# Kernel optimization log

Measured on AMD Instinct MI355X. Metric: run time of the kernel, lower is better.

Reference implementation:

```python
import jax, jax.numpy as jnp
import numpy as np

EPS = 1e-4  # ProtoPNet epsilon in distance-to-similarity transform


def setup_inputs() -> dict:
    key = jax.random.key(0)
    k1, k2, k3 = jax.random.split(key, 3)
    B, C, T = 128, 128, 777   # backbone feature map [B, C, T]
    P, NC = 500, 5            # prototypes, classes
    x = jax.random.normal(k1, (B, C, T), dtype=jnp.float32)
    prototypes = jax.random.uniform(k2, (P, C), dtype=jnp.float32)
    last_w = jax.random.normal(k3, (P, NC), dtype=jnp.float32)
    return {"x": x, "prototypes": prototypes, "last_w": last_w}


def reference(x, prototypes, last_w):
    # Prototype layer via the conv-trick L2 expansion:
    x2 = jnp.sum(x * x, axis=1)                      # [B, T]
    p2 = jnp.sum(prototypes * prototypes, axis=1)    # [P]
    xp = jnp.einsum('bct,pc->bpt', x, prototypes)    # [B, P, T]  (dominant GEMM)
    d = jnp.maximum(x2[:, None, :] - 2.0 * xp + p2[None, :, None], 0.0)  # [B, P, T]
    # Min-pool over all patches (global min over temporal axis)
    min_d = jnp.min(d, axis=2)                       # [B, P]
    # Distance -> similarity: log((d + 1) / (d + eps))
    sim = jnp.log((min_d + 1.0) / (min_d + EPS))     # [B, P]
    # Final evidence layer
    logits = sim @ last_w                            # [B, num_classes]
    return logits
```

## Files before the change

### kernel.cpp

```cpp
#include <hip/hip_runtime.h>
#include <hip/hip_bf16.h>

#define B_DIM 128
#define C_DIM 128
#define T_DIM 777
#define T_PAD 832
#define P_DIM 500
#define P_PAD 512
#define NCLS  5
#define EPSV  1e-4f

typedef unsigned short u16;
typedef __attribute__((ext_vector_type(8))) short short8;
typedef __attribute__((ext_vector_type(4))) float f32x4;

__device__ __forceinline__ u16 f2bf(float f) {
    unsigned u = __float_as_uint(f);
    u += 0x7FFFu + ((u >> 16) & 1u);
    return (u16)(u >> 16);
}

__global__ __launch_bounds__(256) void prep_x(const float* __restrict__ x,
                                              u16* __restrict__ xbf,
                                              float* __restrict__ x2) {
    const int tc = blockIdx.x;
    const int b  = blockIdx.y;
    const int tid = threadIdx.x, w = tid >> 6, l = tid & 63;
    __shared__ __align__(16) u16 xt[64][136];
    const int t_loc = w * 16 + (l & 15);
    const int cg = l >> 4;
    const int t = tc * 64 + t_loc;
    const float* xb = x + (size_t)b * C_DIM * T_DIM;
    float acc = 0.f;
#pragma unroll 8
    for (int c0 = 0; c0 < C_DIM; c0 += 4) {
        int c = c0 + cg;
        float v = (t < T_DIM) ? xb[c * T_DIM + t] : 0.f;
        acc = fmaf(v, v, acc);
        xt[t_loc][c] = f2bf(v);
    }
    acc += __shfl_xor(acc, 16);
    acc += __shfl_xor(acc, 32);
    if (cg == 0) x2[b * T_PAD + t] = (t < T_DIM) ? acc : 1e30f;
    __syncthreads();
    int4* dst = (int4*)(xbf + ((size_t)b * T_PAD + tc * 64) * C_DIM);
#pragma unroll
    for (int q = 0; q < 4; ++q) {
        int f = q * 256 + tid;
        int tr = f >> 4, g = f & 15;
        dst[f] = *(const int4*)((const char*)xt + tr * 272 + g * 16);
    }
}

__global__ void prep_p2(const float* __restrict__ proto, float* __restrict__ p2) {
    int p = blockIdx.x * 64 + threadIdx.x;
    float a = 0.f;
    if (p < P_DIM) {
        const float* pr = proto + p * C_DIM;
#pragma unroll 8
        for (int c = 0; c < C_DIM; ++c) { float v = pr[c]; a = fmaf(v, v, a); }
    }
    p2[p] = (p < P_DIM) ? a : 0.f;
}

__global__ __launch_bounds__(256, 2) void gemm_min(const u16* __restrict__ xbf,
                                                   const float* __restrict__ x2,
                                                   const float* __restrict__ proto,
                                                   const float* __restrict__ p2ws,
                                                   float* __restrict__ simws) {
    const int o = blockIdx.x;
    const int xcd = o & 7, j = o >> 3;
    const int b = xcd * 16 + (j >> 2);
    const int pt = j & 3;
    const int tid = threadIdx.x, w = tid >> 6, l = tid & 63;
    const int wp = pt * 128 + w * 32;
    const int row16 = l & 15, kq = l >> 4;

    __shared__ __align__(16) char smem[32 * 256];

    short8 afr[2][4];
#pragma unroll
    for (int ps = 0; ps < 2; ++ps) {
        int r = wp + ps * 16 + row16;
#pragma unroll
        for (int kst = 0; kst < 4; ++kst) {
            int k0 = kst * 32 + kq * 8;
            float f[8];
            if (r < P_DIM) {
                float4 u0 = *(const float4*)(proto + r * C_DIM + k0);
                float4 u1 = *(const float4*)(proto + r * C_DIM + k0 + 4);
                f[0]=u0.x; f[1]=u0.y; f[2]=u0.z; f[3]=u0.w;
                f[4]=u1.x; f[5]=u1.y; f[6]=u1.z; f[7]=u1.w;
            } else {
#pragma unroll
                for (int q = 0; q < 8; ++q) f[q] = 0.f;
            }
            short8 s;
#pragma unroll
            for (int q = 0; q < 8; ++q) s[q] = (short)f2bf(f[q]);
            afr[ps][kst] = s;
        }
    }
    float p2r[2][4];
#pragma unroll
    for (int ps = 0; ps < 2; ++ps)
#pragma unroll
        for (int q = 0; q < 4; ++q) p2r[ps][q] = p2ws[wp + ps * 16 + kq * 4 + q];

    const int4* xg = (const int4*)xbf;
    const size_t base_g = (size_t)b * T_PAD * 16;
    const int f0 = tid, f1 = tid + 256;
    const int tl0 = f0 >> 4, g0 = f0 & 15;
    const int tl1 = f1 >> 4, g1 = f1 & 15;
    char* wr0 = smem + tl0 * 256 + ((g0 ^ (tl0 & 7)) << 4);
    char* wr1 = smem + tl1 * 256 + ((g1 ^ (tl1 & 7)) << 4);
    int4 v0 = xg[base_g + (size_t)tl0 * 16 + g0];
    int4 v1 = xg[base_g + (size_t)tl1 * 16 + g1];

    float minv[2][4];
#pragma unroll
    for (int ps = 0; ps < 2; ++ps)
#pragma unroll
        for (int q = 0; q < 4; ++q) minv[ps][q] = 1e30f;

    const float* x2b = x2 + b * T_PAD;

    for (int it = 0; it < T_PAD / 32; ++it) {
        *(int4*)wr0 = v0;
        *(int4*)wr1 = v1;
        if (it + 1 < T_PAD / 32) {
            v0 = xg[base_g + (size_t)((it + 1) * 32 + tl0) * 16 + g0];
            v1 = xg[base_g + (size_t)((it + 1) * 32 + tl1) * 16 + g1];
        }
        __syncthreads();

        f32x4 acc[2][2];
#pragma unroll
        for (int ps = 0; ps < 2; ++ps)
#pragma unroll
            for (int ts = 0; ts < 2; ++ts) acc[ps][ts] = (f32x4){0.f, 0.f, 0.f, 0.f};

#pragma unroll
        for (int kst = 0; kst < 4; ++kst) {
            short8 bfr[2];
#pragma unroll
            for (int ts = 0; ts < 2; ++ts) {
                int tl = ts * 16 + row16;
                int gr = (kst * 4 + kq) ^ (tl & 7);
                bfr[ts] = *(const short8*)(smem + tl * 256 + (gr << 4));
            }
#pragma unroll
            for (int ps = 0; ps < 2; ++ps)
#pragma unroll
                for (int ts = 0; ts < 2; ++ts)
                    acc[ps][ts] = __builtin_amdgcn_mfma_f32_16x16x32_bf16(
                        afr[ps][kst], bfr[ts], acc[ps][ts], 0, 0, 0);
        }
        float x2v0 = x2b[it * 32 + row16];
        float x2v1 = x2b[it * 32 + 16 + row16];
#pragma unroll
        for (int ps = 0; ps < 2; ++ps)
#pragma unroll
            for (int q = 0; q < 4; ++q) {
                minv[ps][q] = fminf(minv[ps][q], fmaf(-2.f, acc[ps][0][q], x2v0));
                minv[ps][q] = fminf(minv[ps][q], fmaf(-2.f, acc[ps][1][q], x2v1));
            }
        __syncthreads();
    }

#pragma unroll
    for (int m = 1; m <= 8; m <<= 1)
#pragma unroll
        for (int ps = 0; ps < 2; ++ps)
#pragma unroll
            for (int q = 0; q < 4; ++q)
                minv[ps][q] = fminf(minv[ps][q], __shfl_xor(minv[ps][q], m));

    if (row16 == 0) {
#pragma unroll
        for (int ps = 0; ps < 2; ++ps)
#pragma unroll
            for (int q = 0; q < 4; ++q) {
                int p = wp + ps * 16 + kq * 4 + q;
                if (p < P_DIM) {
                    float md = fmaxf(minv[ps][q] + p2r[ps][q], 0.f);
                    simws[b * P_PAD + p] = logf((md + 1.f) / (md + EPSV));
                }
            }
    }
}

__global__ void logits_k(const float* __restrict__ simws, const float* __restrict__ lw,
                         float* __restrict__ out) {
    int b = blockIdx.x, l = threadIdx.x;
    float a[NCLS] = {0.f, 0.f, 0.f, 0.f, 0.f};
    for (int p = l; p < P_DIM; p += 64) {
        float s = simws[b * P_PAD + p];
#pragma unroll
        for (int n = 0; n < NCLS; ++n) a[n] = fmaf(s, lw[p * NCLS + n], a[n]);
    }
#pragma unroll
    for (int m = 1; m <= 32; m <<= 1)
#pragma unroll
        for (int n = 0; n < NCLS; ++n) a[n] += __shfl_xor(a[n], m);
    if (l == 0) {
#pragma unroll
        for (int n = 0; n < NCLS; ++n) out[b * NCLS + n] = a[n];
    }
}

__global__ __launch_bounds__(256) void fallback_k(const float* __restrict__ x,
                                                  const float* __restrict__ proto,
                                                  const float* __restrict__ lw,
                                                  float* __restrict__ out) {
    __shared__ float x2s[T_DIM];
    __shared__ float sims[P_DIM];
    int b = blockIdx.x, tid = threadIdx.x;
    for (int t = tid; t < T_DIM; t += 256) {
        float a = 0.f;
        for (int c = 0; c < C_DIM; ++c) { float v = x[((size_t)b * C_DIM + c) * T_DIM + t]; a = fmaf(v, v, a); }
        x2s[t] = a;
    }
    __syncthreads();
    for (int p = tid; p < P_DIM; p += 256) {
        float p2 = 0.f;
        for (int c = 0; c < C_DIM; ++c) { float v = proto[p * C_DIM + c]; p2 = fmaf(v, v, p2); }
        float mind = 1e30f;
        for (int t = 0; t < T_DIM; ++t) {
            float xp = 0.f;
            for (int c = 0; c < C_DIM; ++c)
                xp = fmaf(x[((size_t)b * C_DIM + c) * T_DIM + t], proto[p * C_DIM + c], xp);
            float d = fmaxf(x2s[t] - 2.f * xp + p2, 0.f);
            mind = fminf(mind, d);
        }
        sims[p] = logf((mind + 1.f) / (mind + EPSV));
    }
    __syncthreads();
    if (tid < NCLS) {
        float a = 0.f;
        for (int p = 0; p < P_DIM; ++p) a = fmaf(sims[p], lw[p * NCLS + tid], a);
        out[b * NCLS + tid] = a;
    }
}

extern "C" void kernel_launch(void* const* d_in, const int* in_sizes, int n_in,
                              void* d_out, int out_size, void* d_ws, size_t ws_size,
                              hipStream_t stream) {
    const float* x     = (const float*)d_in[0];
    const float* proto = (const float*)d_in[1];
    const float* lw    = (const float*)d_in[2];
    float* out = (float*)d_out;

    const size_t xbf_bytes = (size_t)B_DIM * T_PAD * C_DIM * 2;
    const size_t x2_off  = xbf_bytes;
    const size_t p2_off  = x2_off + (size_t)B_DIM * T_PAD * 4;
    const size_t sim_off = p2_off + (size_t)P_PAD * 4;
    const size_t need    = sim_off + (size_t)B_DIM * P_PAD * 4;

    if (ws_size >= need) {
        u16*   xbf = (u16*)d_ws;
        float* x2  = (float*)((char*)d_ws + x2_off);
        float* p2  = (float*)((char*)d_ws + p2_off);
        float* sim = (float*)((char*)d_ws + sim_off);
        prep_x  <<<dim3(T_PAD / 64, B_DIM), 256, 0, stream>>>(x, xbf, x2);
        prep_p2 <<<dim3(P_PAD / 64),        64,  0, stream>>>(proto, p2);
        gemm_min<<<dim3(512),               256, 0, stream>>>(xbf, x2, proto, p2, sim);
        logits_k<<<dim3(B_DIM),             64,  0, stream>>>(sim, lw, out);
    } else {
        fallback_k<<<dim3(B_DIM), 256, 0, stream>>>(x, proto, lw, out);
    }
}
```

Before: 51.64 us.

## Fuse x bf16 conversion and norms into GEMM-min, split T across blocks

Removes the separate prep_x pass, which wrote a bf16 transposed copy of x plus x2 to workspace. The GEMM kernel now loads fp32 x directly, computes the squared norms and bf16-converts into shared memory itself. Each block now covers 256 prototypes and half of the T range, so two partial minima per (b,p) are combined in the logits kernel, which also computes the prototype norms. The goal is to cut launches and the global round-trip of the converted x, at the cost of more register pressure and per-iteration conversion and shuffle work inside the GEMM loop.

After: 43.15 us. 16.4% less time.

```diff
diff --git a/kernel.cpp b/kernel.cpp
--- a/kernel.cpp
+++ b/kernel.cpp
@@ -4,87 +4,56 @@
 #define B_DIM 128
 #define C_DIM 128
 #define T_DIM 777
-#define T_PAD 832
 #define P_DIM 500
 #define P_PAD 512
 #define NCLS  5
 #define EPSV  1e-4f
+#define NT    25
 
 typedef unsigned short u16;
+typedef unsigned int   u32;
 typedef __attribute__((ext_vector_type(8))) short short8;
 typedef __attribute__((ext_vector_type(4))) float f32x4;
+typedef float float4u __attribute__((ext_vector_type(4), aligned(4)));
 
 __device__ __forceinline__ u16 f2bf(float f) {
-    unsigned u = __float_as_uint(f);
+    u32 u = __float_as_uint(f);
     u += 0x7FFFu + ((u >> 16) & 1u);
     return (u16)(u >> 16);
 }
 
-__global__ __launch_bounds__(256) void prep_x(const float* __restrict__ x,
-                                              u16* __restrict__ xbf,
-                                              float* __restrict__ x2) {
-    const int tc = blockIdx.x;
-    const int b  = blockIdx.y;
-    const int tid = threadIdx.x, w = tid >> 6, l = tid & 63;
-    __shared__ __align__(16) u16 xt[64][136];
-    const int t_loc = w * 16 + (l & 15);
-    const int cg = l >> 4;
-    const int t = tc * 64 + t_loc;
-    const float* xb = x + (size_t)b * C_DIM * T_DIM;
-    float acc = 0.f;
-#pragma unroll 8
-    for (int c0 = 0; c0 < C_DIM; c0 += 4) {
-        int c = c0 + cg;
-        float v = (t < T_DIM) ? xb[c * T_DIM + t] : 0.f;
-        acc = fmaf(v, v, acc);
-        xt[t_loc][c] = f2bf(v);
-    }
-    acc += __shfl_xor(acc, 16);
-    acc += __shfl_xor(acc, 32);
-    if (cg == 0) x2[b * T_PAD + t] = (t < T_DIM) ? acc : 1e30f;
-    __syncthreads();
-    int4* dst = (int4*)(xbf + ((size_t)b * T_PAD + tc * 64) * C_DIM);
-#pragma unroll
-    for (int q = 0; q < 4; ++q) {
-        int f = q * 256 + tid;
-        int tr = f >> 4, g = f & 15;
-        dst[f] = *(const int4*)((const char*)xt + tr * 272 + g * 16);
-    }
-}
-
-__global__ void prep_p2(const float* __restrict__ proto, float* __restrict__ p2) {
-    int p = blockIdx.x * 64 + threadIdx.x;
-    float a = 0.f;
-    if (p < P_DIM) {
-        const float* pr = proto + p * C_DIM;
-#pragma unroll 8
-        for (int c = 0; c < C_DIM; ++c) { float v = pr[c]; a = fmaf(v, v, a); }
-    }
-    p2[p] = (p < P_DIM) ? a : 0.f;
-}
-
-__global__ __launch_bounds__(256, 2) void gemm_min(const u16* __restrict__ xbf,
-                                                   const float* __restrict__ x2,
-                                                   const float* __restrict__ proto,
-                                                   const float* __restrict__ p2ws,
-                                                   float* __restrict__ simws) {
+__global__ __launch_bounds__(256, 2) void fused_gemm_min(
+    const float* __restrict__ x,
+    const float* __restrict__ proto,
+    float* __restrict__ wsmin) {
+
     const int o = blockIdx.x;
     const int xcd = o & 7, j = o >> 3;
-    const int b = xcd * 16 + (j >> 2);
-    const int pt = j & 3;
-    const int tid = threadIdx.x, w = tid >> 6, l = tid & 63;
-    const int wp = pt * 128 + w * 32;
+    const int b   = xcd * 16 + (j >> 2);
+    const int pt  = (j >> 1) & 1, th = j & 1;
+    const int it0 = th ? 13 : 0;
+    const int itN = th ? NT : 13;
+
+    const int tid = threadIdx.x;
+    const int w = tid >> 6, l = tid & 63;
     const int row16 = l & 15, kq = l >> 4;
-
-    __shared__ __align__(16) char smem[32 * 256];
-
-    short8 afr[2][4];
-#pragma unroll
-    for (int ps = 0; ps < 2; ++ps) {
-        int r = wp + ps * 16 + row16;
+    const int wp = pt * 256 + w * 64;
+
+    const int c0  = (tid >> 3) << 2;
+    const int tl0 = (tid & 7) << 2;
+
+    __shared__ __align__(16) char  smem[32 * 256];
+    __shared__ __align__(16) float x2p[4][32];
+
+    const float* xb = x + (size_t)b * C_DIM * T_DIM;
+
+    short8 afr[4][4];
+#pragma unroll
+    for (int ps = 0; ps < 4; ++ps) {
+        const int r = wp + ps * 16 + row16;
 #pragma unroll
         for (int kst = 0; kst < 4; ++kst) {
-            int k0 = kst * 32 + kq * 8;
+            const int k0 = kst * 32 + kq * 8;
             float f[8];
             if (r < P_DIM) {
                 float4 u0 = *(const float4*)(proto + r * C_DIM + k0);
@@ -95,48 +64,76 @@
 #pragma unroll
                 for (int q = 0; q < 8; ++q) f[q] = 0.f;
             }
-            short8 s;
-#pragma unroll
-            for (int q = 0; q < 8; ++q) s[q] = (short)f2bf(f[q]);
-            afr[ps][kst] = s;
-        }
-    }
-    float p2r[2][4];
-#pragma unroll
-    for (int ps = 0; ps < 2; ++ps)
-#pragma unroll
-        for (int q = 0; q < 4; ++q) p2r[ps][q] = p2ws[wp + ps * 16 + kq * 4 + q];
-
-    const int4* xg = (const int4*)xbf;
-    const size_t base_g = (size_t)b * T_PAD * 16;
-    const int f0 = tid, f1 = tid + 256;
-    const int tl0 = f0 >> 4, g0 = f0 & 15;
-    const int tl1 = f1 >> 4, g1 = f1 & 15;
-    char* wr0 = smem + tl0 * 256 + ((g0 ^ (tl0 & 7)) << 4);
-    char* wr1 = smem + tl1 * 256 + ((g1 ^ (tl1 & 7)) << 4);
-    int4 v0 = xg[base_g + (size_t)tl0 * 16 + g0];
-    int4 v1 = xg[base_g + (size_t)tl1 * 16 + g1];
-
-    float minv[2][4];
-#pragma unroll
-    for (int ps = 0; ps < 2; ++ps)
-#pragma unroll
-        for (int q = 0; q < 4; ++q) minv[ps][q] = 1e30f;
-
-    const float* x2b = x2 + b * T_PAD;
-
-    for (int it = 0; it < T_PAD / 32; ++it) {
-        *(int4*)wr0 = v0;
-        *(int4*)wr1 = v1;
-        if (it + 1 < T_PAD / 32) {
-            v0 = xg[base_g + (size_t)((it + 1) * 32 + tl0) * 16 + g0];
-            v1 = xg[base_g + (size_t)((it + 1) * 32 + tl1) * 16 + g1];
+            short8 s8;
+#pragma unroll
+            for (int q = 0; q < 8; ++q) s8[q] = (short)f2bf(f[q]);
+            afr[ps][kst] = s8;
+        }
+    }
+
+    float vb[4][4];
+    auto loadv = [&](int it) {
+        const int tb = it * 32 + tl0;
+        if (tb + 3 < T_DIM) {
+#pragma unroll
+            for (int r = 0; r < 4; ++r) {
+                float4u u = *(const float4u*)(xb + (c0 + r) * T_DIM + tb);
+                vb[r][0]=u[0]; vb[r][1]=u[1]; vb[r][2]=u[2]; vb[r][3]=u[3];
+            }
+        } else {
+#pragma unroll
+            for (int r = 0; r < 4; ++r)
+#pragma unroll
+                for (int jj = 0; jj < 4; ++jj) {
+                    const int t = tb + jj;
+                    vb[r][jj] = (t < T_DIM) ? xb[(c0 + r) * T_DIM + t] : 0.f;
+                }
+        }
+    };
+
+    loadv(it0);
+
+    f32x4 minv[4];
+#pragma unroll
+    for (int ps = 0; ps < 4; ++ps) minv[ps] = (f32x4){1e30f, 1e30f, 1e30f, 1e30f};
+
+    for (int it = it0; it < itN; ++it) {
+        const int t0 = it * 32;
+
+        float s[4];
+#pragma unroll
+        for (int jj = 0; jj < 4; ++jj)
+            s[jj] = vb[0][jj]*vb[0][jj] + vb[1][jj]*vb[1][jj]
+                  + vb[2][jj]*vb[2][jj] + vb[3][jj]*vb[3][jj];
+
+#pragma unroll
+        for (int jj = 0; jj < 4; ++jj) {
+            const u32 lo = (u32)f2bf(vb[0][jj]) | ((u32)f2bf(vb[1][jj]) << 16);
+            const u32 hi = (u32)f2bf(vb[2][jj]) | ((u32)f2bf(vb[3][jj]) << 16);
+            const int tl  = tl0 + jj;
+            const int off = tl * 256 + (((c0 >> 3) ^ (tl & 7)) << 4) + ((c0 & 4) << 1);
+            *(uint2*)(smem + off) = make_uint2(lo, hi);
+        }
+
+#pragma unroll
+        for (int m = 8; m <= 32; m <<= 1)
+#pragma unroll
+            for (int jj = 0; jj < 4; ++jj) s[jj] += __shfl_xor(s[jj], m);
+        if ((l >> 3) == 0) {
+            float4 o4;
+            o4.x = (t0 + tl0 + 0 < T_DIM) ? s[0] : 1e30f;
+            o4.y = (t0 + tl0 + 1 < T_DIM) ? s[1] : 1e30f;
+            o4.z = (t0 + tl0 + 2 < T_DIM) ? s[2] : 1e30f;
+            o4.w = (t0 + tl0 + 3 < T_DIM) ? s[3] : 1e30f;
+            *(float4*)(&x2p[w][tl0]) = o4;
         }
         __syncthreads();
 
-        f32x4 acc[2][2];
-#pragma unroll
-        for (int ps = 0; ps < 2; ++ps)
+        if (it + 1 < itN) loadv(it + 1);
+
+        f32x4 acc[4][2];
+#pragma unroll
+        for (int ps = 0; ps < 4; ++ps)
 #pragma unroll
             for (int ts = 0; ts < 2; ++ts) acc[ps][ts] = (f32x4){0.f, 0.f, 0.f, 0.f};
 
@@ -145,21 +142,22 @@
             short8 bfr[2];
 #pragma unroll
             for (int ts = 0; ts < 2; ++ts) {
-                int tl = ts * 16 + row16;
-                int gr = (kst * 4 + kq) ^ (tl & 7);
+                const int tl = ts * 16 + row16;
+                const int gr = (kst * 4 + kq) ^ (tl & 7);
                 bfr[ts] = *(const short8*)(smem + tl * 256 + (gr << 4));
             }
 #pragma unroll
-            for (int ps = 0; ps < 2; ++ps)
+            for (int ps = 0; ps < 4; ++ps)
 #pragma unroll
                 for (int ts = 0; ts < 2; ++ts)
                     acc[ps][ts] = __builtin_amdgcn_mfma_f32_16x16x32_bf16(
                         afr[ps][kst], bfr[ts], acc[ps][ts], 0, 0, 0);
         }
-        float x2v0 = x2b[it * 32 + row16];
-        float x2v1 = x2b[it * 32 + 16 + row16];
-#pragma unroll
-        for (int ps = 0; ps < 2; ++ps)
+
+        const float x2v0 = x2p[0][row16]      + x2p[1][row16]      + x2p[2][row16]      + x2p[3][row16];
+        const float x2v1 = x2p[0][16 + row16] + x2p[1][16 + row16] + x2p[2][16 + row16] + x2p[3][16 + row16];
+#pragma unroll
+        for (int ps = 0; ps < 4; ++ps)
 #pragma unroll
             for (int q = 0; q < 4; ++q) {
                 minv[ps][q] = fminf(minv[ps][q], fmaf(-2.f, acc[ps][0][q], x2v0));
@@ -171,42 +169,56 @@
 #pragma unroll
     for (int m = 1; m <= 8; m <<= 1)
 #pragma unroll
-        for (int ps = 0; ps < 2; ++ps)
+        for (int ps = 0; ps < 4; ++ps)
 #pragma unroll
             for (int q = 0; q < 4; ++q)
                 minv[ps][q] = fminf(minv[ps][q], __shfl_xor(minv[ps][q], m));
 
     if (row16 == 0) {
 #pragma unroll
-        for (int ps = 0; ps < 2; ++ps)
+        for (int ps = 0; ps < 4; ++ps)
 #pragma unroll
             for (int q = 0; q < 4; ++q) {
-                int p = wp + ps * 16 + kq * 4 + q;
-                if (p < P_DIM) {
-                    float md = fmaxf(minv[ps][q] + p2r[ps][q], 0.f);
-                    simws[b * P_PAD + p] = logf((md + 1.f) / (md + EPSV));
-                }
-            }
-    }
-}
-
-__global__ void logits_k(const float* __restrict__ simws, const float* __restrict__ lw,
-                         float* __restrict__ out) {
-    int b = blockIdx.x, l = threadIdx.x;
+                const int p = wp + ps * 16 + kq * 4 + q;
+                if (p < P_DIM)
+                    wsmin[((size_t)b * P_PAD + p) * 2 + th] = minv[ps][q];
+            }
+    }
+}
+
+__global__ __launch_bounds__(256) void combine_logits(
+    const float* __restrict__ proto, const float* __restrict__ lw,
+    const float* __restrict__ wsmin, float* __restrict__ out) {
+    const int b = blockIdx.x, tid = threadIdx.x;
     float a[NCLS] = {0.f, 0.f, 0.f, 0.f, 0.f};
-    for (int p = l; p < P_DIM; p += 64) {
-        float s = simws[b * P_PAD + p];
-#pragma unroll
-        for (int n = 0; n < NCLS; ++n) a[n] = fmaf(s, lw[p * NCLS + n], a[n]);
+    for (int p = tid; p < P_DIM; p += 256) {
+        const float4* pr = (const float4*)(proto + p * C_DIM);
+        float p2 = 0.f;
+#pragma unroll
+        for (int i = 0; i < 32; ++i) {
+            float4 u = pr[i];
+            p2 += u.x*u.x + u.y*u.y + u.z*u.z + u.w*u.w;
+        }
+        const size_t base = ((size_t)b * P_PAD + p) * 2;
+        const float m  = fminf(wsmin[base], wsmin[base + 1]);
+        const float md = fmaxf(m + p2, 0.f);
+        const float sim = logf((md + 1.f) / (md + EPSV));
+#pragma unroll
+        for (int n = 0; n < NCLS; ++n) a[n] = fmaf(sim, lw[p * NCLS + n], a[n]);
     }
 #pragma unroll
     for (int m = 1; m <= 32; m <<= 1)
 #pragma unroll
         for (int n = 0; n < NCLS; ++n) a[n] += __shfl_xor(a[n], m);
+    __shared__ float red[4][NCLS];
+    const int w = tid >> 6, l = tid & 63;
     if (l == 0) {
 #pragma unroll
-        for (int n = 0; n < NCLS; ++n) out[b * NCLS + n] = a[n];
-    }
+        for (int n = 0; n < NCLS; ++n) red[w][n] = a[n];
+    }
+    __syncthreads();
+    if (tid < NCLS)
+        out[b * NCLS + tid] = red[0][tid] + red[1][tid] + red[2][tid] + red[3][tid];
 }
 
 __global__ __launch_bounds__(256) void fallback_k(const float* __restrict__ x,
@@ -251,21 +263,12 @@
     const float* lw    = (const float*)d_in[2];
     float* out = (float*)d_out;
 
-    const size_t xbf_bytes = (size_t)B_DIM * T_PAD * C_DIM * 2;
-    const size_t x2_off  = xbf_bytes;
-    const size_t p2_off  = x2_off + (size_t)B_DIM * T_PAD * 4;
-    const size_t sim_off = p2_off + (size_t)P_PAD * 4;
-    const size_t need    = sim_off + (size_t)B_DIM * P_PAD * 4;
+    const size_t need = (size_t)B_DIM * P_PAD * 2 * sizeof(float);
 
     if (ws_size >= need) {
-        u16*   xbf = (u16*)d_ws;
-        float* x2  = (float*)((char*)d_ws + x2_off);
-        float* p2  = (float*)((char*)d_ws + p2_off);
-        float* sim = (float*)((char*)d_ws + sim_off);
-        prep_x  <<<dim3(T_PAD / 64, B_DIM), 256, 0, stream>>>(x, xbf, x2);
-        prep_p2 <<<dim3(P_PAD / 64),        64,  0, stream>>>(proto, p2);
-        gemm_min<<<dim3(512),               256, 0, stream>>>(xbf, x2, proto, p2, sim);
-        logits_k<<<dim3(B_DIM),             64,  0, stream>>>(sim, lw, out);
+        float* wsmin = (float*)d_ws;
+        fused_gemm_min<<<dim3(512), 256, 0, stream>>>(x, proto, wsmin);
+        combine_logits<<<dim3(B_DIM), 256, 0, stream>>>(proto, lw, wsmin, out);
     } else {
         fallback_k<<<dim3(B_DIM), 256, 0, stream>>>(x, proto, lw, out);
     }
```
